# Optimization experiments

Measured on AMD Instinct MI355X. Metric: run time of the kernel, lower is better.

The kernel has to match this reference:

```python
import jax, jax.numpy as jnp
import numpy as np

N = 2000   # nodes
K = 16     # receptive-field size (exact degree incl. self-loop)
C_IN = 16  # input_feats
H = 16     # hidden_size
NC = 18    # num_contractions


def setup_inputs() -> dict:
    key = jax.random.key(0)
    k1, k2, k3, k4, k5, k6 = jax.random.split(key, 6)
    # adjacency with exactly K ones per row (self-loop + K-1 distinct random nbrs)
    u = jax.random.uniform(k1, (N, N))
    u = u.at[jnp.arange(N), jnp.arange(N)].set(-1.0)  # force self into top-K
    nbrs = jnp.argsort(u, axis=1)[:, :K]
    adj = jnp.zeros((N, N), jnp.float32).at[jnp.arange(N)[:, None], nbrs].set(1.0)
    X = jax.random.normal(k2, (N, C_IN), jnp.float32)
    scale = 0.1
    W1 = scale * jax.random.normal(k3, (H, NC * C_IN), jnp.float32)
    b1 = jnp.zeros((H,), jnp.float32)
    W2 = scale * jax.random.normal(k4, (H, NC * H), jnp.float32)
    b2 = jnp.zeros((H,), jnp.float32)
    fc_w = scale * jax.random.normal(k5, (1, 2 * H + C_IN), jnp.float32)
    fc_b = scale * jax.random.normal(k6, (1,), jnp.float32)
    return {"X": X, "adj": adj, "W1": W1, "b1": b1, "W2": W2, "b2": b2,
            "fc_w": fc_w, "fc_b": fc_b}


def _neighbors(adj):
    # each row has exactly K ones -> top_k returns their indices
    _, idx = jax.lax.top_k(adj, K)
    return jnp.sort(idx, axis=1)  # (N, K)


def _contract18(T):
    # T: (n, m, a, b, c) stacked promoted neighbor tensors; 18 contractions 3rd->2nd order
    n, k, _, _, c = T.shape
    tr = lambda M: jnp.swapaxes(M, 1, 2)
    s0, s1, s2 = T.sum(1), T.sum(2), T.sum(3)           # single-index sums
    d0 = jnp.einsum('ixxbc->ixbc', T)                    # diag m=a
    d1 = jnp.einsum('ixaxc->ixac', T)                    # diag m=b
    d2 = jnp.einsum('imyyc->imyc', T)                    # diag a=b
    outs = []
    for M in (s0, s1, s2, d0, d1, d2):
        outs.append(M)
        outs.append(tr(M))                               # 12 so far
    v0, v1, v2 = T.sum((2, 3)), T.sum((1, 3)), T.sum((1, 2))  # double sums -> vectors
    for v in (v0, v1, v2):
        outs.append(jnp.broadcast_to(v[:, :, None, :], (n, k, k, c)))  # rows
        outs.append(jnp.broadcast_to(v[:, None, :, :], (n, k, k, c)))  # cols
    return jnp.concatenate(outs, axis=-1)                # (n, k, k, 18c)


def _forward(X, adj, W1, b1, W2, b2, fc_w, fc_b):
    nbrs = _neighbors(adj)                               # (N, K)
    nbrs_nb = nbrs[nbrs]                                 # (N, K, K)
    # chi[i,m,a,b] = 1 iff a-th member of P_i equals b-th member of P_{nbrs[i,m]}
    chi = (nbrs[:, None, :, None] == nbrs_nb[:, :, None, :]).astype(X.dtype)  # (N,K,K,K)
    # F0: first->second order promotion (features on the diagonal of P_i x P_i)
    F0 = jnp.einsum('ab,iac->iabc', jnp.eye(K, dtype=X.dtype), X[nbrs])  # (N,K,K,C_IN)

    def step(F, W, b):
        Fn = F[nbrs]                                     # (N, m, p, q, c)
        tmp = jnp.einsum('imap,impqc->imaqc', chi, Fn)
        T = jnp.einsum('imaqc,imbq->imabc', tmp, chi)    # promoted + stacked (N,m,a,b,c)
        C = _contract18(T)                               # (N, a, b, 18c)
        return jax.nn.relu(jnp.einsum('iabk,hk->iabh', C, W) + b)

    F1 = step(F0, W1, b1)
    F2 = step(F1, W2, b2)
    g = jnp.concatenate([F0.sum((0, 1, 2)), F1.sum((0, 1, 2)), F2.sum((0, 1, 2))])
    return g @ fc_w.T + fc_b                             # (n_outputs,)


def reference(X, adj, W1, b1, W2, b2, fc_w, fc_b):
    return _forward(X, adj, W1, b1, W2, b2, fc_w, fc_b)
```

## Files before the change

kernel.cpp:

```cpp
#include <hip/hip_runtime.h>

#define NN 2000

typedef _Float16 halfx8 __attribute__((ext_vector_type(8)));
typedef float floatx4 __attribute__((ext_vector_type(4)));

#define LBAR() asm volatile("s_waitcnt lgkmcnt(0)\n\ts_barrier" ::: "memory")

__global__ void build_nbrs_k(const float* __restrict__ adj,
                             int* __restrict__ nbrs) {
    int i = blockIdx.x;
    int lane = threadIdx.x;
    const float* row = adj + (size_t)i * NN;
    int base = 0;
    for (int chunk = 0; chunk < (NN + 63) / 64; ++chunk) {
        int col = chunk * 64 + lane;
        float a = (col < NN) ? row[col] : 0.0f;
        bool p = a > 0.5f;
        unsigned long long mask = __ballot(p);
        if (p) {
            int pos = base + __popcll(mask & ((1ull << lane) - 1ull));
            nbrs[i * 16 + pos] = col;
        }
        base += __popcll(mask);
    }
}

__global__ void build_map_k(const int* __restrict__ nbrs,
                            signed char* __restrict__ map8,
                            signed char* __restrict__ imp8) {
    int idx = blockIdx.x * blockDim.x + threadIdx.x;
    if (idx >= NN * 16) return;
    int i = idx >> 4;
    int j = nbrs[idx];
    const int4* pi = (const int4*)(nbrs + i * 16);
    const int4* pj = (const int4*)(nbrs + (size_t)j * 16);
    int4 A = pi[0], Bq = pi[1], C = pi[2], D = pi[3];
    int4 E = pj[0], F = pj[1], G = pj[2], H = pj[3];
    int ni[16] = {A.x,A.y,A.z,A.w, Bq.x,Bq.y,Bq.z,Bq.w, C.x,C.y,C.z,C.w, D.x,D.y,D.z,D.w};
    int nj[16] = {E.x,E.y,E.z,E.w, F.x,F.y,F.z,F.w, G.x,G.y,G.z,G.w, H.x,H.y,H.z,H.w};
    unsigned long long lo = 0, hi = 0;
#pragma unroll
    for (int a = 0; a < 16; ++a) {
        int r = -1;
#pragma unroll
        for (int p = 0; p < 16; ++p)
            if (nj[p] == ni[a]) r = p;
        unsigned long long b = (unsigned long long)(r & 0xff);
        if (a < 8) lo |= b << (8 * a); else hi |= b << (8 * (a - 8));
    }
    uint4 pk;
    pk.x = (unsigned)lo; pk.y = (unsigned)(lo >> 32);
    pk.z = (unsigned)hi; pk.w = (unsigned)(hi >> 32);
    *(uint4*)(map8 + ((size_t)idx << 4)) = pk;
    lo = 0; hi = 0;
#pragma unroll
    for (int p = 0; p < 16; ++p) {
        int r = -1;
#pragma unroll
        for (int a = 0; a < 16; ++a)
            if (ni[a] == nj[p]) r = a;
        unsigned long long b = (unsigned long long)(r & 0xff);
        if (p < 8) lo |= b << (8 * p); else hi |= b << (8 * (p - 8));
    }
    pk.x = (unsigned)lo; pk.y = (unsigned)(lo >> 32);
    pk.z = (unsigned)hi; pk.w = (unsigned)(hi >> 32);
    *(uint4*)(imp8 + ((size_t)idx << 4)) = pk;
}

__global__ void prep_w_k(const float* __restrict__ W1,
                         const float* __restrict__ W2,
                         _Float16* __restrict__ Wpk) {
    int idx = blockIdx.x * blockDim.x + threadIdx.x;
    if (idx >= 2 * 10 * 512) return;
    int stage = idx / 5120;
    int rem = idx % 5120;
    int chunk = rem / 512;
    int r2 = rem % 512;
    int L = r2 / 8, j = r2 % 8;
    int q = L >> 4, h = L & 15;
    int k = q * 8 + j;
    const int tA[10] = {0, 4, 8, 12, 16, 1, 5, 9, 13, 17};
    const int tB[10] = {2, 6, 10, 14, -1, 3, 7, 11, 15, -1};
    int tblk = (k < 16) ? tA[chunk] : tB[chunk];
    int c = k & 15;
    const float* W = stage ? W2 : W1;
    float val = (tblk < 0) ? 0.f : W[h * 288 + tblk * 16 + c];
    Wpk[idx] = (_Float16)val;
}

template <int DIAG>
__global__ __launch_bounds__(256, 2)
void step_k(const float* __restrict__ Fp,
            const float* __restrict__ Xp,
            const _Float16* __restrict__ Wpk,
            const float* __restrict__ bias,
            const int* __restrict__ nbrs,
            const signed char* __restrict__ map8,
            const signed char* __restrict__ imp8,
            float* __restrict__ Fout,
            float* __restrict__ gp0,
            float* __restrict__ gp) {
    __shared__ __attribute__((aligned(16))) float S0[16][16][18];
    __shared__ __attribute__((aligned(16))) _Float16 MAP[5][16][16][16];
    __shared__ __attribute__((aligned(16))) float V0f[16][16];
    __shared__ __attribute__((aligned(16))) float V1f[16][16];
    __shared__ __attribute__((aligned(16))) float V2f[16][16];
    __shared__ __attribute__((aligned(16))) float S1f[16][16];

    const int i = blockIdx.x;
    const int t = threadIdx.x;
    const int u = t >> 4;
    const int l = t & 15;
    const int lane = t & 63, q = lane >> 4, h = lane & 15, wv = t >> 6;

    float frow[16], fcol[16], xv = 0.f;
    if (!DIAG) {
        const float* Fi = Fp + (size_t)i * 4096;
#pragma unroll
        for (int b = 0; b < 16; ++b) frow[b] = Fi[(u * 16 + b) * 16 + l];
#pragma unroll
        for (int a = 0; a < 16; ++a) fcol[a] = Fi[(a * 16 + u) * 16 + l];
    }
    const int4* nbp = (const int4*)(nbrs + (size_t)i * 16);
    int4 nA = nbp[0], nB = nbp[1], nC = nbp[2], nD = nbp[3];
    const int j = nbrs[(size_t)i * 16 + u];
    uint4 mpq = *(const uint4*)(map8 + ((size_t)(i * 16 + u) << 4));
    uint4 imv = *(const uint4*)(imp8 + ((size_t)(i * 16 + u) << 4));
    float bv = bias[l];

    int ms = 0;
    {
        int nn[16] = {nA.x,nA.y,nA.z,nA.w, nB.x,nB.y,nB.z,nB.w,
                      nC.x,nC.y,nC.z,nC.w, nD.x,nD.y,nD.z,nD.w};
#pragma unroll
        for (int m2 = 0; m2 < 16; ++m2)
            if (nn[m2] == i) ms = m2;
    }
    if (DIAG) xv = Xp[(size_t)j * 16 + l];

    unsigned vm = 0;
    int a1 = -1, a2 = -1, pa1 = 0, pa2 = 0;
#pragma unroll
    for (int a = 0; a < 16; ++a) {
        unsigned dw = (a < 4) ? mpq.x : ((a < 8) ? mpq.y : ((a < 12) ? mpq.z : mpq.w));
        int pa = (int)(signed char)((dw >> (8 * (a & 3))) & 0xffu);
        if (pa >= 0) {
            vm |= (1u << a);
            if (a1 < 0)      { a1 = a; pa1 = pa; }
            else if (a2 < 0) { a2 = a; pa2 = pa; }
        }
    }
    int pmm;
    {
        unsigned dw = (u & 8) ? ((u & 4) ? mpq.w : mpq.z) : ((u & 4) ? mpq.y : mpq.x);
        pmm = (int)(signed char)((dw >> (8 * (u & 3))) & 0xffu);
    }

    float R1[16], R2[16];
    if (!DIAG && u != ms) {
        const float* P1 = Fp + (((size_t)j * 256 + pa1 * 16) * 16) + l;
#pragma unroll
        for (int p = 0; p < 16; ++p) R1[p] = P1[p * 16];
        if (a2 >= 0) {
            const float* P2 = Fp + (((size_t)j * 256 + pa2 * 16) * 16) + l;
#pragma unroll
            for (int p = 0; p < 16; ++p) R2[p] = P2[p * 16];
        }
    }

    if (u != ms) {
        uint4 z = {0u, 0u, 0u, 0u};
#pragma unroll
        for (int k = 0; k < 5; ++k) {
            *(uint4*)&MAP[k][u][l][0] = z;
            *(uint4*)&MAP[k][u][l][8] = z;
        }
    }
    if (DIAG) {
        S1f[u][l] = xv;
        V1f[u][l] = xv;
        V2f[u][l] = xv;
#pragma unroll
        for (int b = 0; b < 16; ++b) S0[u][b][l] = (b == u) ? xv : 0.f;
        MAP[0][ms][u][l] = (_Float16)xv;
        MAP[1][ms][u][l] = (_Float16)xv;
        _Float16 dz = (_Float16)((u == ms) ? xv : 0.f);
        MAP[2][ms][u][l] = dz;
        MAP[3][ms][u][l] = dz;
        MAP[4][ms][u][l] = (_Float16)xv;
    } else {
        float s2 = 0.f, a10 = 0.f, a8 = 0.f;
#pragma unroll
        for (int b = 0; b < 16; ++b) {
            float v = frow[b];
            s2 += v;
            S0[u][b][l] = v;
            if (b == u)  a10 = v;
            if (b == ms) a8 = v;
        }
        float s1 = 0.f, a6 = 0.f;
#pragma unroll
        for (int a = 0; a < 16; ++a) {
            float v = fcol[a];
            s1 += v;
            if (a == ms) a6 = v;
        }
        S1f[u][l] = s2;
        V1f[u][l] = s2;
        V2f[u][l] = s1;
        MAP[0][ms][u][l] = (_Float16)s1;
        MAP[1][ms][u][l] = (_Float16)s2;
        MAP[2][ms][u][l] = (_Float16)a6;
        MAP[3][ms][u][l] = (_Float16)a8;
        MAP[4][ms][u][l] = (_Float16)a10;
    }
    LBAR();

    if (u != ms) {
        const int m = u;
        float v0acc = 0.f;
        if (DIAG) {
#pragma unroll
            for (int a = 0; a < 16; ++a) {
                unsigned dw = (a < 4) ? mpq.x : ((a < 8) ? mpq.y : ((a < 12) ? mpq.z : mpq.w));
                int pa = (int)(signed char)((dw >> (8 * (a & 3))) & 0xffu);
                if (pa >= 0) {
                    float v = S1f[a][l];
                    v0acc += v;
                    atomicAdd(&S0[a][a][l], v);
                    atomicAdd(&V1f[a][l], v);
                    atomicAdd(&V2f[a][l], v);
                    MAP[0][m][a][l] = (_Float16)v;
                    MAP[1][m][a][l] = (_Float16)v;
                    MAP[4][m][a][l] = (_Float16)v;
                    if (a == m) { MAP[2][m][m][l] = (_Float16)v; MAP[3][m][m][l] = (_Float16)v; }
                }
            }
        } else {
            float colacc[16];
#pragma unroll
            for (int p = 0; p < 16; ++p) colacc[p] = 0.f;
            auto process = [&](int a, int pa, const float (&vr)[16]) {
                float rowacc = 0.f, a8v = 0.f, a10v = 0.f;
                const bool am = (a == m);
#pragma unroll
                for (int p = 0; p < 16; ++p) {
                    float v = vr[p];
                    if (p == pmm) a8v = v;
                    if (p == pa)  a10v = v;
                    unsigned dw = (p < 4) ? imv.x : ((p < 8) ? imv.y : ((p < 12) ? imv.z : imv.w));
                    int b = (int)(signed char)((dw >> (8 * (p & 3))) & 0xffu);
                    if (b >= 0) {
                        rowacc += v;
                        colacc[p] += v;
                        atomicAdd(&S0[a][b][l], v);
                        atomicAdd(&V2f[b][l], v);
                        if (am) MAP[2][m][b][l] = (_Float16)v;
                    }
                }
                v0acc += rowacc;
                atomicAdd(&V1f[a][l], rowacc);
                MAP[1][m][a][l] = (_Float16)rowacc;
                MAP[3][m][a][l] = (_Float16)a8v;
                MAP[4][m][a][l] = (_Float16)a10v;
            };
            process(a1, pa1, R1);
            if (a2 >= 0) process(a2, pa2, R2);
            unsigned rm = vm & ~(1u << a1);
            if (a2 >= 0) rm &= ~(1u << a2);
            while (rm) {
                int a = __builtin_ctz(rm); rm &= rm - 1;
                unsigned dw = (a & 8) ? ((a & 4) ? mpq.w : mpq.z) : ((a & 4) ? mpq.y : mpq.x);
                int pa = (int)(signed char)((dw >> (8 * (a & 3))) & 0xffu);
                float RT[16];
                const float* P3 = Fp + (((size_t)j * 256 + pa * 16) * 16) + l;
#pragma unroll
                for (int p = 0; p < 16; ++p) RT[p] = P3[p * 16];
                process(a, pa, RT);
            }
            V0f[m][l] = v0acc;
#pragma unroll
            for (int p = 0; p < 16; ++p) {
                unsigned dw = (p < 4) ? imv.x : ((p < 8) ? imv.y : ((p < 12) ? imv.z : imv.w));
                int b = (int)(signed char)((dw >> (8 * (p & 3))) & 0xffu);
                if (b >= 0) MAP[0][m][b][l] = (_Float16)colacc[p];
            }
        }
        if (DIAG) V0f[m][l] = v0acc;
    } else {
        float v0s = 0.f;
#pragma unroll
        for (int b = 0; b < 16; ++b) v0s += S1f[b][l];
        V0f[ms][l] = v0s;
        if (DIAG) gp0[(size_t)i * 16 + l] = v0s;
    }

    halfx8 B[10];
    {
        const halfx8* Wp8 = (const halfx8*)Wpk;
#pragma unroll
        for (int c = 0; c < 10; ++c) B[c] = Wp8[c * 64 + lane];
    }
    LBAR();

    halfx8 az;
#pragma unroll
    for (int z = 0; z < 8; ++z) az[z] = (_Float16)0.f;
    auto cvt8 = [](const float* p) -> halfx8 {
        float2 fa = *(const float2*)p, fb = *(const float2*)(p + 2),
               fc = *(const float2*)(p + 4), fd = *(const float2*)(p + 6);
        halfx8 r;
        r[0] = (_Float16)fa.x; r[1] = (_Float16)fa.y; r[2] = (_Float16)fb.x; r[3] = (_Float16)fb.y;
        r[4] = (_Float16)fc.x; r[5] = (_Float16)fc.y; r[6] = (_Float16)fd.x; r[7] = (_Float16)fd.y;
        return r;
    };
    auto cvt8a = [](const float* p) -> halfx8 {
        float4 va = *(const float4*)p, vb = *(const float4*)(p + 4);
        halfx8 r;
        r[0] = (_Float16)va.x; r[1] = (_Float16)va.y; r[2] = (_Float16)va.z; r[3] = (_Float16)va.w;
        r[4] = (_Float16)vb.x; r[5] = (_Float16)vb.y; r[6] = (_Float16)vb.z; r[7] = (_Float16)vb.w;
        return r;
    };

    floatx4 acc1[4], acc2[4];
#pragma unroll
    for (int tt = 0; tt < 4; ++tt) {
        acc1[tt] = (floatx4){0.f, 0.f, 0.f, 0.f};
        acc2[tt] = (floatx4){0.f, 0.f, 0.f, 0.f};
    }
    const int wbase = wv * 4;
#pragma unroll
    for (int tt = 0; tt < 4; ++tt) {
        const int x = wbase + tt;
        halfx8 af0, af1, af2, af3, af4;
        if (q < 2) {
            af0 = cvt8(&S0[x][h][q * 8]);
            af1 = *(const halfx8*)&MAP[1][x][h][q * 8];
            af2 = *(const halfx8*)&MAP[3][x][h][q * 8];
            af3 = cvt8a(&V0f[x][q * 8]);
            af4 = cvt8a(&V2f[x][q * 8]);
        } else {
            const int c0 = (q - 2) * 8;
            af0 = *(const halfx8*)&MAP[0][x][h][c0];
            af1 = *(const halfx8*)&MAP[2][x][h][c0];
            af2 = *(const halfx8*)&MAP[4][x][h][c0];
            af3 = cvt8a(&V1f[x][c0]);
            af4 = az;
        }
        acc1[tt] = __builtin_amdgcn_mfma_f32_16x16x32_f16(af0, B[0], acc1[tt], 0, 0, 0);
        acc1[tt] = __builtin_amdgcn_mfma_f32_16x16x32_f16(af1, B[1], acc1[tt], 0, 0, 0);
        acc1[tt] = __builtin_amdgcn_mfma_f32_16x16x32_f16(af2, B[2], acc1[tt], 0, 0, 0);
        acc1[tt] = __builtin_amdgcn_mfma_f32_16x16x32_f16(af3, B[3], acc1[tt], 0, 0, 0);
        acc1[tt] = __builtin_amdgcn_mfma_f32_16x16x32_f16(af4, B[4], acc1[tt], 0, 0, 0);
        acc2[tt] = __builtin_amdgcn_mfma_f32_16x16x32_f16(af0, B[5], acc2[tt], 0, 0, 0);
        acc2[tt] = __builtin_amdgcn_mfma_f32_16x16x32_f16(af1, B[6], acc2[tt], 0, 0, 0);
        acc2[tt] = __builtin_amdgcn_mfma_f32_16x16x32_f16(af2, B[7], acc2[tt], 0, 0, 0);
        acc2[tt] = __builtin_amdgcn_mfma_f32_16x16x32_f16(af3, B[8], acc2[tt], 0, 0, 0);
        acc2[tt] = __builtin_amdgcn_mfma_f32_16x16x32_f16(af4, B[9], acc2[tt], 0, 0, 0);
    }
    LBAR();

    float* P2f = &S0[0][0][0];
#pragma unroll
    for (int tt = 0; tt < 4; ++tt) {
        const int x = wbase + tt;
#pragma unroll
        for (int r = 0; r < 4; ++r)
            P2f[(x * 16 + (q * 4 + r)) * 17 + h] = acc2[tt][r];
    }
    LBAR();

    float gpart = 0.f;
#pragma unroll
    for (int tt = 0; tt < 4; ++tt) {
        const int x = wbase + tt;
#pragma unroll
        for (int r = 0; r < 4; ++r) {
            const int y = q * 4 + r;
            float val = acc1[tt][r] + P2f[(y * 16 + x) * 17 + h] + bv;
            val = fmaxf(val, 0.f);
            gpart += val;
            if (Fout) Fout[(size_t)i * 4096 + (x * 16 + y) * 16 + h] = val;
        }
    }
    gpart += __shfl_xor(gpart, 16, 64);
    gpart += __shfl_xor(gpart, 32, 64);
    if (lane < 16) S1f[wv][h] = gpart;
    LBAR();
    if (t < 16) gp[(size_t)i * 16 + t] = S1f[0][t] + S1f[1][t] + S1f[2][t] + S1f[3][t];
}

__global__ void reduce_g_k(const float* __restrict__ parts,
                           float* __restrict__ gsum) {
    int r = blockIdx.x;
    int stage = r >> 4, h = r & 15;
    const float* p = parts + (size_t)stage * NN * 16 + h;
    int t = threadIdx.x;
    float s = 0.f;
    for (int n = t; n < NN; n += 256) s += p[(size_t)n * 16];
#pragma unroll
    for (int off = 32; off > 0; off >>= 1) s += __shfl_xor(s, off, 64);
    __shared__ float wsum[4];
    if ((t & 63) == 0) wsum[t >> 6] = s;
    __syncthreads();
    if (t == 0) gsum[r] = wsum[0] + wsum[1] + wsum[2] + wsum[3];
}

__global__ void finalize_k(const float* __restrict__ gsum,
                           const float* __restrict__ fcw,
                           const float* __restrict__ fcb,
                           float* __restrict__ out) {
    int t = threadIdx.x;
    float v = (t < 48) ? gsum[t] * fcw[t] : 0.f;
#pragma unroll
    for (int off = 32; off > 0; off >>= 1) v += __shfl_xor(v, off, 64);
    if (t == 0) out[0] = v + fcb[0];
}

extern "C" void kernel_launch(void* const* d_in, const int* in_sizes, int n_in,
                              void* d_out, int out_size, void* d_ws, size_t ws_size,
                              hipStream_t stream) {
    const float* X   = (const float*)d_in[0];
    const float* adj = (const float*)d_in[1];
    const float* W1  = (const float*)d_in[2];
    const float* b1  = (const float*)d_in[3];
    const float* W2  = (const float*)d_in[4];
    const float* b2  = (const float*)d_in[5];
    const float* fcw = (const float*)d_in[6];
    const float* fcb = (const float*)d_in[7];
    float* out = (float*)d_out;
    char* ws = (char*)d_ws;

    float*       gsum  = (float*)(ws + 0);
    int*         nbrs  = (int*)(ws + 1024);
    signed char* map8  = (signed char*)(ws + 129280);
    signed char* imp8  = (signed char*)(ws + 641280);
    float*       parts = (float*)(ws + 1153280);
    _Float16*    Wpk   = (_Float16*)(ws + 1537280);
    float*       F1    = (float*)(ws + 1557760);

    build_nbrs_k<<<NN, 64, 0, stream>>>(adj, nbrs);
    build_map_k<<<(NN * 16 + 255) / 256, 256, 0, stream>>>(nbrs, map8, imp8);
    prep_w_k<<<40, 256, 0, stream>>>(W1, W2, Wpk);
    step_k<1><<<NN, 256, 0, stream>>>(nullptr, X, Wpk, b1, nbrs, map8, imp8, F1,
                                      parts, parts + (size_t)1 * NN * 16);
    step_k<0><<<NN, 256, 0, stream>>>(F1, X, Wpk + 5120, b2, nbrs, map8, imp8, nullptr,
                                      nullptr, parts + (size_t)2 * NN * 16);
    reduce_g_k<<<48, 256, 0, stream>>>(parts, gsum);
    finalize_k<<<1, 64, 0, stream>>>(gsum, fcw, fcb, out);
}
```

Before: 167.1 us.

## Precompute per-edge aux metadata, split MFMA to overlap LDS, drop final barrier

build_map_k now emits a packed per-edge aux record (neighbor id, first two matches, valid mask, diagonal index, self slot), so the step kernel no longer loads the neighbor list or decodes the map itself. The weight blocks are permuted so the MFMAs that read only MAP data can run before the barrier that publishes S0/V sums, and the weight fragments are loaded earlier. The per-block graph sum is written per wave, which removes a barrier but makes the reduction read four times more partials. build_nbrs_k also preloads all adjacency chunks before the ballot loop to raise memory-level parallelism, at the cost of more registers.

```diff
diff --git a/kernel.cpp b/kernel.cpp
--- a/kernel.cpp
+++ b/kernel.cpp
@@ -12,15 +12,20 @@
     int i = blockIdx.x;
     int lane = threadIdx.x;
     const float* row = adj + (size_t)i * NN;
+    float v[32];
+#pragma unroll
+    for (int c = 0; c < 32; ++c) {
+        int col = c * 64 + lane;
+        v[c] = (col < NN) ? row[col] : 0.0f;
+    }
     int base = 0;
-    for (int chunk = 0; chunk < (NN + 63) / 64; ++chunk) {
-        int col = chunk * 64 + lane;
-        float a = (col < NN) ? row[col] : 0.0f;
-        bool p = a > 0.5f;
+#pragma unroll
+    for (int c = 0; c < 32; ++c) {
+        bool p = v[c] > 0.5f;
         unsigned long long mask = __ballot(p);
         if (p) {
             int pos = base + __popcll(mask & ((1ull << lane) - 1ull));
-            nbrs[i * 16 + pos] = col;
+            nbrs[i * 16 + pos] = c * 64 + lane;
         }
         base += __popcll(mask);
     }
@@ -28,17 +33,21 @@
 
 __global__ void build_map_k(const int* __restrict__ nbrs,
                             signed char* __restrict__ map8,
-                            signed char* __restrict__ imp8) {
+                            signed char* __restrict__ imp8,
+                            int4* __restrict__ aux) {
     int idx = blockIdx.x * blockDim.x + threadIdx.x;
     if (idx >= NN * 16) return;
     int i = idx >> 4;
+    int m = idx & 15;
     int j = nbrs[idx];
-    const int4* pi = (const int4*)(nbrs + i * 16);
+    const int4* pi = (const int4*)(nbrs + (size_t)i * 16);
     const int4* pj = (const int4*)(nbrs + (size_t)j * 16);
     int4 A = pi[0], Bq = pi[1], C = pi[2], D = pi[3];
     int4 E = pj[0], F = pj[1], G = pj[2], H = pj[3];
     int ni[16] = {A.x,A.y,A.z,A.w, Bq.x,Bq.y,Bq.z,Bq.w, C.x,C.y,C.z,C.w, D.x,D.y,D.z,D.w};
     int nj[16] = {E.x,E.y,E.z,E.w, F.x,F.y,F.z,F.w, G.x,G.y,G.z,G.w, H.x,H.y,H.z,H.w};
+
+    int mp[16];
     unsigned long long lo = 0, hi = 0;
 #pragma unroll
     for (int a = 0; a < 16; ++a) {
@@ -46,6 +55,7 @@
 #pragma unroll
         for (int p = 0; p < 16; ++p)
             if (nj[p] == ni[a]) r = p;
+        mp[a] = r;
         unsigned long long b = (unsigned long long)(r & 0xff);
         if (a < 8) lo |= b << (8 * a); else hi |= b << (8 * (a - 8));
     }
@@ -66,6 +76,27 @@
     pk.x = (unsigned)lo; pk.y = (unsigned)(lo >> 32);
     pk.z = (unsigned)hi; pk.w = (unsigned)(hi >> 32);
     *(uint4*)(imp8 + ((size_t)idx << 4)) = pk;
+
+    unsigned vm = 0;
+    int a1 = -1, a2 = -1, pa1 = 0, pa2 = 0;
+#pragma unroll
+    for (int a = 0; a < 16; ++a) {
+        if (mp[a] >= 0) {
+            vm |= (1u << a);
+            if (a1 < 0)      { a1 = a; pa1 = mp[a]; }
+            else if (a2 < 0) { a2 = a; pa2 = mp[a]; }
+        }
+    }
+    int ms = 0;
+#pragma unroll
+    for (int a = 0; a < 16; ++a)
+        if (ni[a] == i) ms = a;
+    int4 av;
+    av.x = j;
+    av.y = (a1 & 0xff) | ((pa1 & 0xff) << 8) | ((a2 & 0xff) << 16) | ((pa2 & 0xff) << 24);
+    av.z = (int)(vm | ((unsigned)(mp[m] & 0xff) << 16) | ((unsigned)(ms & 0xff) << 24));
+    av.w = 0;
+    aux[idx] = av;
 }
 
 __global__ void prep_w_k(const float* __restrict__ W1,
@@ -77,11 +108,11 @@
     int rem = idx % 5120;
     int chunk = rem / 512;
     int r2 = rem % 512;
-    int L = r2 / 8, j = r2 % 8;
+    int L = r2 / 8, jj = r2 % 8;
     int q = L >> 4, h = L & 15;
-    int k = q * 8 + j;
-    const int tA[10] = {0, 4, 8, 12, 16, 1, 5, 9, 13, 17};
-    const int tB[10] = {2, 6, 10, 14, -1, 3, 7, 11, 15, -1};
+    int k = q * 8 + jj;
+    const int tA[10] = {2, 6, 10, 0, 14,   3, 7, 11, 1, 15};
+    const int tB[10] = {4, 8, -1, 12, 16,  5, 9, -1, 13, 17};
     int tblk = (k < 16) ? tA[chunk] : tB[chunk];
     int c = k & 15;
     const float* W = stage ? W2 : W1;
@@ -95,9 +126,9 @@
             const float* __restrict__ Xp,
             const _Float16* __restrict__ Wpk,
             const float* __restrict__ bias,
-            const int* __restrict__ nbrs,
             const signed char* __restrict__ map8,
             const signed char* __restrict__ imp8,
+            const int4* __restrict__ auxp,
             float* __restrict__ Fout,
             float* __restrict__ gp0,
             float* __restrict__ gp) {
@@ -114,47 +145,27 @@
     const int l = t & 15;
     const int lane = t & 63, q = lane >> 4, h = lane & 15, wv = t >> 6;
 
-    float frow[16], fcol[16], xv = 0.f;
-    if (!DIAG) {
-        const float* Fi = Fp + (size_t)i * 4096;
-#pragma unroll
-        for (int b = 0; b < 16; ++b) frow[b] = Fi[(u * 16 + b) * 16 + l];
-#pragma unroll
-        for (int a = 0; a < 16; ++a) fcol[a] = Fi[(a * 16 + u) * 16 + l];
-    }
-    const int4* nbp = (const int4*)(nbrs + (size_t)i * 16);
-    int4 nA = nbp[0], nB = nbp[1], nC = nbp[2], nD = nbp[3];
-    const int j = nbrs[(size_t)i * 16 + u];
-    uint4 mpq = *(const uint4*)(map8 + ((size_t)(i * 16 + u) << 4));
+    int4 av = auxp[i * 16 + u];
     uint4 imv = *(const uint4*)(imp8 + ((size_t)(i * 16 + u) << 4));
     float bv = bias[l];
-
-    int ms = 0;
-    {
-        int nn[16] = {nA.x,nA.y,nA.z,nA.w, nB.x,nB.y,nB.z,nB.w,
-                      nC.x,nC.y,nC.z,nC.w, nD.x,nD.y,nD.z,nD.w};
-#pragma unroll
-        for (int m2 = 0; m2 < 16; ++m2)
-            if (nn[m2] == i) ms = m2;
-    }
-    if (DIAG) xv = Xp[(size_t)j * 16 + l];
-
-    unsigned vm = 0;
-    int a1 = -1, a2 = -1, pa1 = 0, pa2 = 0;
-#pragma unroll
-    for (int a = 0; a < 16; ++a) {
-        unsigned dw = (a < 4) ? mpq.x : ((a < 8) ? mpq.y : ((a < 12) ? mpq.z : mpq.w));
-        int pa = (int)(signed char)((dw >> (8 * (a & 3))) & 0xffu);
-        if (pa >= 0) {
-            vm |= (1u << a);
-            if (a1 < 0)      { a1 = a; pa1 = pa; }
-            else if (a2 < 0) { a2 = a; pa2 = pa; }
-        }
-    }
-    int pmm;
-    {
-        unsigned dw = (u & 8) ? ((u & 4) ? mpq.w : mpq.z) : ((u & 4) ? mpq.y : mpq.x);
-        pmm = (int)(signed char)((dw >> (8 * (u & 3))) & 0xffu);
+    const int j = av.x;
+    const int a1 = (int)(signed char)(av.y & 0xff);
+    const int pa1 = (av.y >> 8) & 0xff;
+    const int a2 = (int)(signed char)((av.y >> 16) & 0xff);
+    const int pa2 = (av.y >> 24) & 0xff;
+    const unsigned vm = (unsigned)(av.z & 0xffff);
+    const int pmm = (av.z >> 16) & 0xff;
+    const int ms = (av.z >> 24) & 0xff;
+
+    float frow[16], fcol[16], xv = 0.f;
+    if (DIAG) {
+        xv = Xp[(size_t)j * 16 + l];
+    } else {
+        const float* Fi = Fp + (size_t)i * 4096;
+#pragma unroll
+        for (int b = 0; b < 16; ++b) frow[b] = Fi[(u * 16 + b) * 16 + l];
+#pragma unroll
+        for (int a = 0; a < 16; ++a) fcol[a] = Fi[(a * 16 + u) * 16 + l];
     }
 
     float R1[16], R2[16];
@@ -167,6 +178,12 @@
 #pragma unroll
             for (int p = 0; p < 16; ++p) R2[p] = P2[p * 16];
         }
+    }
+    halfx8 B[10];
+    {
+        const halfx8* Wp8 = (const halfx8*)Wpk;
+#pragma unroll
+        for (int c = 0; c < 10; ++c) B[c] = Wp8[c * 64 + lane];
     }
 
     if (u != ms) {
@@ -223,9 +240,7 @@
         if (DIAG) {
 #pragma unroll
             for (int a = 0; a < 16; ++a) {
-                unsigned dw = (a < 4) ? mpq.x : ((a < 8) ? mpq.y : ((a < 12) ? mpq.z : mpq.w));
-                int pa = (int)(signed char)((dw >> (8 * (a & 3))) & 0xffu);
-                if (pa >= 0) {
+                if ((vm >> a) & 1u) {
                     float v = S1f[a][l];
                     v0acc += v;
                     atomicAdd(&S0[a][a][l], v);
@@ -269,17 +284,19 @@
             if (a2 >= 0) process(a2, pa2, R2);
             unsigned rm = vm & ~(1u << a1);
             if (a2 >= 0) rm &= ~(1u << a2);
-            while (rm) {
-                int a = __builtin_ctz(rm); rm &= rm - 1;
-                unsigned dw = (a & 8) ? ((a & 4) ? mpq.w : mpq.z) : ((a & 4) ? mpq.y : mpq.x);
-                int pa = (int)(signed char)((dw >> (8 * (a & 3))) & 0xffu);
-                float RT[16];
-                const float* P3 = Fp + (((size_t)j * 256 + pa * 16) * 16) + l;
-#pragma unroll
-                for (int p = 0; p < 16; ++p) RT[p] = P3[p * 16];
-                process(a, pa, RT);
+            if (rm) {
+                uint4 mpq = *(const uint4*)(map8 + ((size_t)(i * 16 + u) << 4));
+                do {
+                    int a = __builtin_ctz(rm); rm &= rm - 1;
+                    unsigned dw = (a & 8) ? ((a & 4) ? mpq.w : mpq.z) : ((a & 4) ? mpq.y : mpq.x);
+                    int pa = (int)(signed char)((dw >> (8 * (a & 3))) & 0xffu);
+                    float RT[16];
+                    const float* P3 = Fp + (((size_t)j * 256 + pa * 16) * 16) + l;
+#pragma unroll
+                    for (int p = 0; p < 16; ++p) RT[p] = P3[p * 16];
+                    process(a, pa, RT);
+                } while (rm);
             }
-            V0f[m][l] = v0acc;
 #pragma unroll
             for (int p = 0; p < 16; ++p) {
                 unsigned dw = (p < 4) ? imv.x : ((p < 8) ? imv.y : ((p < 12) ? imv.z : imv.w));
@@ -287,7 +304,7 @@
                 if (b >= 0) MAP[0][m][b][l] = (_Float16)colacc[p];
             }
         }
-        if (DIAG) V0f[m][l] = v0acc;
+        V0f[m][l] = v0acc;
     } else {
         float v0s = 0.f;
 #pragma unroll
@@ -296,17 +313,39 @@
         if (DIAG) gp0[(size_t)i * 16 + l] = v0s;
     }
 
-    halfx8 B[10];
-    {
-        const halfx8* Wp8 = (const halfx8*)Wpk;
-#pragma unroll
-        for (int c = 0; c < 10; ++c) B[c] = Wp8[c * 64 + lane];
+    floatx4 acc1[4], acc2[4];
+#pragma unroll
+    for (int tt = 0; tt < 4; ++tt) {
+        acc1[tt] = (floatx4){0.f, 0.f, 0.f, 0.f};
+        acc2[tt] = (floatx4){0.f, 0.f, 0.f, 0.f};
+    }
+    halfx8 az;
+#pragma unroll
+    for (int z = 0; z < 8; ++z) az[z] = (_Float16)0.f;
+    const int wbase = wv * 4;
+#pragma unroll
+    for (int tt = 0; tt < 4; ++tt) {
+        const int x = wbase + tt;
+        halfx8 p0, p1, p2;
+        if (q < 2) {
+            p0 = *(const halfx8*)&MAP[0][x][h][q * 8];
+            p1 = *(const halfx8*)&MAP[2][x][h][q * 8];
+            p2 = *(const halfx8*)&MAP[4][x][h][q * 8];
+        } else {
+            const int c0 = (q - 2) * 8;
+            p0 = *(const halfx8*)&MAP[1][x][h][c0];
+            p1 = *(const halfx8*)&MAP[3][x][h][c0];
+            p2 = az;
+        }
+        acc1[tt] = __builtin_amdgcn_mfma_f32_16x16x32_f16(p0, B[0], acc1[tt], 0, 0, 0);
+        acc1[tt] = __builtin_amdgcn_mfma_f32_16x16x32_f16(p1, B[1], acc1[tt], 0, 0, 0);
+        acc1[tt] = __builtin_amdgcn_mfma_f32_16x16x32_f16(p2, B[2], acc1[tt], 0, 0, 0);
+        acc2[tt] = __builtin_amdgcn_mfma_f32_16x16x32_f16(p0, B[5], acc2[tt], 0, 0, 0);
+        acc2[tt] = __builtin_amdgcn_mfma_f32_16x16x32_f16(p1, B[6], acc2[tt], 0, 0, 0);
+        acc2[tt] = __builtin_amdgcn_mfma_f32_16x16x32_f16(p2, B[7], acc2[tt], 0, 0, 0);
     }
     LBAR();
 
-    halfx8 az;
-#pragma unroll
-    for (int z = 0; z < 8; ++z) az[z] = (_Float16)0.f;
     auto cvt8 = [](const float* p) -> halfx8 {
         float2 fa = *(const float2*)p, fb = *(const float2*)(p + 2),
                fc = *(const float2*)(p + 4), fd = *(const float2*)(p + 6);
@@ -322,42 +361,22 @@
         r[4] = (_Float16)vb.x; r[5] = (_Float16)vb.y; r[6] = (_Float16)vb.z; r[7] = (_Float16)vb.w;
         return r;
     };
-
-    floatx4 acc1[4], acc2[4];
-#pragma unroll
-    for (int tt = 0; tt < 4; ++tt) {
-        acc1[tt] = (floatx4){0.f, 0.f, 0.f, 0.f};
-        acc2[tt] = (floatx4){0.f, 0.f, 0.f, 0.f};
-    }
-    const int wbase = wv * 4;
 #pragma unroll
     for (int tt = 0; tt < 4; ++tt) {
         const int x = wbase + tt;
-        halfx8 af0, af1, af2, af3, af4;
+        halfx8 p3, p4;
         if (q < 2) {
-            af0 = cvt8(&S0[x][h][q * 8]);
-            af1 = *(const halfx8*)&MAP[1][x][h][q * 8];
-            af2 = *(const halfx8*)&MAP[3][x][h][q * 8];
-            af3 = cvt8a(&V0f[x][q * 8]);
-            af4 = cvt8a(&V2f[x][q * 8]);
+            p3 = cvt8(&S0[x][h][q * 8]);
+            p4 = cvt8a(&V1f[x][q * 8]);
         } else {
             const int c0 = (q - 2) * 8;
-            af0 = *(const halfx8*)&MAP[0][x][h][c0];
-            af1 = *(const halfx8*)&MAP[2][x][h][c0];
-            af2 = *(const halfx8*)&MAP[4][x][h][c0];
-            af3 = cvt8a(&V1f[x][c0]);
-            af4 = az;
-        }
-        acc1[tt] = __builtin_amdgcn_mfma_f32_16x16x32_f16(af0, B[0], acc1[tt], 0, 0, 0);
-        acc1[tt] = __builtin_amdgcn_mfma_f32_16x16x32_f16(af1, B[1], acc1[tt], 0, 0, 0);
-        acc1[tt] = __builtin_amdgcn_mfma_f32_16x16x32_f16(af2, B[2], acc1[tt], 0, 0, 0);
-        acc1[tt] = __builtin_amdgcn_mfma_f32_16x16x32_f16(af3, B[3], acc1[tt], 0, 0, 0);
-        acc1[tt] = __builtin_amdgcn_mfma_f32_16x16x32_f16(af4, B[4], acc1[tt], 0, 0, 0);
-        acc2[tt] = __builtin_amdgcn_mfma_f32_16x16x32_f16(af0, B[5], acc2[tt], 0, 0, 0);
-        acc2[tt] = __builtin_amdgcn_mfma_f32_16x16x32_f16(af1, B[6], acc2[tt], 0, 0, 0);
-        acc2[tt] = __builtin_amdgcn_mfma_f32_16x16x32_f16(af2, B[7], acc2[tt], 0, 0, 0);
-        acc2[tt] = __builtin_amdgcn_mfma_f32_16x16x32_f16(af3, B[8], acc2[tt], 0, 0, 0);
-        acc2[tt] = __builtin_amdgcn_mfma_f32_16x16x32_f16(af4, B[9], acc2[tt], 0, 0, 0);
+            p3 = cvt8a(&V0f[x][c0]);
+            p4 = cvt8a(&V2f[x][c0]);
+        }
+        acc1[tt] = __builtin_amdgcn_mfma_f32_16x16x32_f16(p3, B[3], acc1[tt], 0, 0, 0);
+        acc1[tt] = __builtin_amdgcn_mfma_f32_16x16x32_f16(p4, B[4], acc1[tt], 0, 0, 0);
+        acc2[tt] = __builtin_amdgcn_mfma_f32_16x16x32_f16(p3, B[8], acc2[tt], 0, 0, 0);
+        acc2[tt] = __builtin_amdgcn_mfma_f32_16x16x32_f16(p4, B[9], acc2[tt], 0, 0, 0);
     }
     LBAR();
 
@@ -386,19 +405,21 @@
     }
     gpart += __shfl_xor(gpart, 16, 64);
     gpart += __shfl_xor(gpart, 32, 64);
-    if (lane < 16) S1f[wv][h] = gpart;
-    LBAR();
-    if (t < 16) gp[(size_t)i * 16 + t] = S1f[0][t] + S1f[1][t] + S1f[2][t] + S1f[3][t];
+    if (lane < 16) gp[((size_t)i * 4 + wv) * 16 + h] = gpart;
 }
 
 __global__ void reduce_g_k(const float* __restrict__ parts,
                            float* __restrict__ gsum) {
     int r = blockIdx.x;
-    int stage = r >> 4, h = r & 15;
-    const float* p = parts + (size_t)stage * NN * 16 + h;
+    int h = r & 15;
+    const float* p;
+    int cnt;
+    if (r < 16)      { p = parts + h;                     cnt = NN; }
+    else if (r < 32) { p = parts + NN * 16 + h;           cnt = NN * 4; }
+    else             { p = parts + NN * 16 + NN * 64 + h; cnt = NN * 4; }
     int t = threadIdx.x;
     float s = 0.f;
-    for (int n = t; n < NN; n += 256) s += p[(size_t)n * 16];
+    for (int n = t; n < cnt; n += 256) s += p[(size_t)n * 16];
 #pragma unroll
     for (int off = 32; off > 0; off >>= 1) s += __shfl_xor(s, off, 64);
     __shared__ float wsum[4];
@@ -436,17 +457,18 @@
     int*         nbrs  = (int*)(ws + 1024);
     signed char* map8  = (signed char*)(ws + 129280);
     signed char* imp8  = (signed char*)(ws + 641280);
-    float*       parts = (float*)(ws + 1153280);
-    _Float16*    Wpk   = (_Float16*)(ws + 1537280);
-    float*       F1    = (float*)(ws + 1557760);
+    int4*        aux   = (int4*)(ws + 1153280);
+    float*       parts = (float*)(ws + 1665280);
+    _Float16*    Wpk   = (_Float16*)(ws + 2817280);
+    float*       F1    = (float*)(ws + 2837760);
 
     build_nbrs_k<<<NN, 64, 0, stream>>>(adj, nbrs);
-    build_map_k<<<(NN * 16 + 255) / 256, 256, 0, stream>>>(nbrs, map8, imp8);
+    build_map_k<<<(NN * 16 + 255) / 256, 256, 0, stream>>>(nbrs, map8, imp8, aux);
     prep_w_k<<<40, 256, 0, stream>>>(W1, W2, Wpk);
-    step_k<1><<<NN, 256, 0, stream>>>(nullptr, X, Wpk, b1, nbrs, map8, imp8, F1,
-                                      parts, parts + (size_t)1 * NN * 16);
-    step_k<0><<<NN, 256, 0, stream>>>(F1, X, Wpk + 5120, b2, nbrs, map8, imp8, nullptr,
-                                      nullptr, parts + (size_t)2 * NN * 16);
+    step_k<1><<<NN, 256, 0, stream>>>(nullptr, X, Wpk, b1, map8, imp8, aux, F1,
+                                      parts, parts + (size_t)NN * 16);
+    step_k<0><<<NN, 256, 0, stream>>>(F1, X, Wpk + 5120, b2, map8, imp8, aux, nullptr,
+                                      nullptr, parts + (size_t)NN * 16 + (size_t)NN * 64);
     reduce_g_k<<<48, 256, 0, stream>>>(parts, gsum);
     finalize_k<<<1, 64, 0, stream>>>(gsum, fcw, fcb, out);
 }
```

After: 165.1 us. About the same (-1.2%).
